# Kernel optimization log

Measured on AMD Instinct MI355X. Metric: run time of the kernel, lower is better.

## Reference

```python
import jax, jax.numpy as jnp
import numpy as np

H, INNER, V = 64, 32, 64
LR = 0.05
B, L = 256, 2048


def setup_inputs() -> dict:
    key = jax.random.key(0)
    ks = jax.random.split(key, 8)
    s = 0.05
    return {
        "seq":   jax.random.randint(ks[0], (B, L), 0, V),
        "embed": jax.random.normal(ks[1], (V, H), jnp.float32) * s,
        "ffw1":  jax.random.normal(ks[2], (2 * H, H), jnp.float32) * s,
        "ffb1":  jnp.zeros((2 * H,), jnp.float32),
        "ffw2":  jax.random.normal(ks[3], (H, 2 * H), jnp.float32) * s,
        "ffb2":  jnp.zeros((H,), jnp.float32),
        "ln_g":  jnp.ones((H,), jnp.float32),
        "ln_b":  jnp.zeros((H,), jnp.float32),
        "w1":    jax.random.normal(ks[4], (INNER, H), jnp.float32) * s,
        "b1":    jnp.zeros((INNER,), jnp.float32),
        "w2":    jax.random.normal(ks[5], (H, INNER), jnp.float32) * s,
        "b2":    jnp.zeros((H,), jnp.float32),
        "wout":  jax.random.normal(ks[6], (V, H), jnp.float32) * s,
        "bout":  jnp.zeros((V,), jnp.float32),
    }


def _encoder(seq, embed, ffw1, ffb1, ffw2, ffb2, ln_g, ln_b):
    e = embed[seq]                                             # [B,L,H]
    ff = jnp.maximum(e @ ffw1.T + ffb1, 0.0) @ ffw2.T + ffb2   # [B,L,H]
    x = e + ff
    mu = x.mean(-1, keepdims=True)
    var = x.var(-1, keepdims=True)                             # biased, like nn.LayerNorm
    return (x - mu) / jnp.sqrt(var + 1e-5) * ln_g + ln_b


def _ttt_one(kseq, vseq, last, w1, b1, w2, b2):
    # Sequential inner-loop TTT: per (k,v) pair, one SGD step on the tiny MLP
    # with analytic gradients of MSE(pred, v) (mean over H).
    def step(carry, kv):
        w1c, b1c, w2c, b2c = carry
        k, v = kv
        pre = w1c @ k + b1c                # [INNER]
        h = jnp.maximum(pre, 0.0)
        pred = w2c @ h + b2c               # [H]
        d = (2.0 / H) * (pred - v)         # dL/dpred
        gw2 = jnp.outer(d, h)
        gb2 = d
        dh = (w2c.T @ d) * (pre > 0.0)
        gw1 = jnp.outer(dh, k)
        gb1 = dh
        return (w1c - LR * gw1, b1c - LR * gb1,
                w2c - LR * gw2, b2c - LR * gb2), None

    (w1f, b1f, w2f, b2f), _ = jax.lax.scan(step, (w1, b1, w2, b2), (kseq, vseq))
    return w2f @ jnp.maximum(w1f @ last + b1f, 0.0) + b2f


def reference(seq, embed, ffw1, ffb1, ffw2, ffb2, ln_g, ln_b,
              w1, b1, w2, b2, wout, bout):
    hs = _encoder(seq, embed, ffw1, ffb1, ffw2, ffb2, ln_g, ln_b)
    hs = jax.lax.stop_gradient(hs)         # torch detaches kh/vh/last
    Lc = hs.shape[1]
    nsteps = (Lc - 2) // 2                 # len(range(0, L-3, 2))
    kseq = hs[:, 0:Lc - 3:2]               # [B,nsteps,H]
    vseq = hs[:, 1:Lc - 2:2][:, :nsteps]   # [B,nsteps,H]
    w1_0 = jax.lax.stop_gradient(w1)
    b1_0 = jax.lax.stop_gradient(b1)
    w2_0 = jax.lax.stop_gradient(w2)
    b2_0 = jax.lax.stop_gradient(b2)
    ctxs = jax.vmap(_ttt_one, in_axes=(0, 0, 0, None, None, None, None))(
        kseq, vseq, hs[:, -1], w1_0, b1_0, w2_0, b2_0)  # [B,H]
    return ctxs @ wout.T + bout            # [B,V]
```

## Files before the change

### kernel.cpp

```cpp
#include <hip/hip_runtime.h>

#define HD 64
#define VOCAB 64
#define BATCH 256
#define SEQLEN 2048
#define NSTEPS ((SEQLEN - 2) / 2)
#define LRc 0.05f

typedef __attribute__((ext_vector_type(2))) float f2;

__device__ __forceinline__ float xsum32(float x) {
  unsigned int u = __float_as_uint(x);
  auto r = __builtin_amdgcn_permlane32_swap(u, u, false, false);
  return __uint_as_float(r[0]) + __uint_as_float(r[1]);
}

__device__ __forceinline__ void pk_fma_s(f2& acc, const f2& w, const f2& shp) {
  asm("v_pk_fma_f32 %0, %2, %1, %0" : "+v"(acc) : "v"(w), "s"(shp));
}

__global__ __launch_bounds__(64, 1) void enc_build(
    const float* __restrict__ embed, const float* __restrict__ ffw1,
    const float* __restrict__ ffb1, const float* __restrict__ ffw2,
    const float* __restrict__ ffb2, const float* __restrict__ ln_g,
    const float* __restrict__ ln_b, float* __restrict__ enc) {
  const int v = blockIdx.x, j = threadIdx.x;
  __shared__ float e_s[HD];
  __shared__ float hid_s[2 * HD];
  float e = embed[v * HD + j];
  e_s[j] = e;
  __syncthreads();
  float ha = ffb1[j], hb = ffb1[HD + j];
  #pragma unroll 8
  for (int h = 0; h < HD; ++h) {
    float eh = e_s[h];
    ha = fmaf(ffw1[j * HD + h], eh, ha);
    hb = fmaf(ffw1[(HD + j) * HD + h], eh, hb);
  }
  hid_s[j] = fmaxf(ha, 0.f);
  hid_s[HD + j] = fmaxf(hb, 0.f);
  __syncthreads();
  float ff = ffb2[j];
  #pragma unroll 8
  for (int h2 = 0; h2 < 2 * HD; ++h2) ff = fmaf(ffw2[j * 2 * HD + h2], hid_s[h2], ff);
  float x = e + ff;
  float mu = x;
  #pragma unroll
  for (int m = 1; m < 64; m <<= 1) mu += __shfl_xor(mu, m, 64);
  mu *= (1.f / 64.f);
  float xc = x - mu;
  float var = xc * xc;
  #pragma unroll
  for (int m = 1; m < 64; m <<= 1) var += __shfl_xor(var, m, 64);
  var *= (1.f / 64.f);
  enc[v * HD + j] = xc / sqrtf(var + 1e-5f) * ln_g[j] + ln_b[j];
}

__global__ __launch_bounds__(64, 1) void gram_build(
    const float* __restrict__ enc, float* __restrict__ G) {
  __shared__ float es[VOCAB * HD];
  const int u = blockIdx.x, v = threadIdx.x;
  #pragma unroll
  for (int q = 0; q < 16; ++q)
    ((float4*)es)[v + 64 * q] = ((const float4*)enc)[v + 64 * q];
  __syncthreads();
  const float* a = &es[u * HD];
  const float* bb = &es[v * HD];
  float s0 = 0.f, s1 = 0.f, s2 = 0.f, s3 = 0.f;
  #pragma unroll
  for (int j = 0; j < HD; j += 4) {
    s0 = fmaf(a[j + 0], bb[j + 0], s0);
    s1 = fmaf(a[j + 1], bb[j + 1], s1);
    s2 = fmaf(a[j + 2], bb[j + 2], s2);
    s3 = fmaf(a[j + 3], bb[j + 3], s3);
  }
  G[u * VOCAB + v] = (s0 + s1) + (s2 + s3);
}

__device__ __forceinline__ void ttt_step(
    int l, int half,
    const float* __restrict__ enc_s, const float* __restrict__ G_s,
    const int* __restrict__ seq_s, float* __restrict__ sd_s,
    f2 (&W1)[16], f2 (&W2R2)[16], f2 (&W2T)[16],
    float& b1r, float& b2r,
    f2 (&KC)[16], float& vvC, f2 (&KN)[16], float& vvN,
    float& POFb, float& KKF, float& dhp,
    int2& tk, int2& tk1, int pidx) {
  float pre = fmaf(dhp, KKF, POFb);
  float h = fmaxf(pre, 0.f);

  const float* krn = &enc_s[tk1.x * HD + half * 32];
  float4* kn4 = (float4*)&KN[0];
  #pragma unroll
  for (int q = 0; q < 8; ++q) kn4[q] = *(const float4*)&krn[4 * q];
  vvN = enc_s[tk1.y * HD + l];
  float KKFn = G_s[tk.x * VOCAB + tk1.x];
  int2 tk2 = *(const int2*)&seq_s[pidx];

  f2 shp[16];
  #pragma unroll
  for (int c = 0; c < 16; ++c) {
    float a = __int_as_float(__builtin_amdgcn_readlane(__float_as_int(h), 2 * c));
    float bq = __int_as_float(__builtin_amdgcn_readlane(__float_as_int(h), 2 * c + 1));
    shp[c] = f2{a, bq};
  }

  f2 qa = {b2r, 0.f}, qb = {0.f, 0.f}, qc = {0.f, 0.f}, qd = {0.f, 0.f};
  #pragma unroll
  for (int c = 0; c < 16; c += 4) {
    pk_fma_s(qa, W2R2[c + 0], shp[c + 0]);
    pk_fma_s(qb, W2R2[c + 1], shp[c + 1]);
    pk_fma_s(qc, W2R2[c + 2], shp[c + 2]);
    pk_fma_s(qd, W2R2[c + 3], shp[c + 3]);
  }
  float pred = ((qa.x + qa.y) + (qb.x + qb.y)) + ((qc.x + qc.y) + (qd.x + qd.y));
  float sR = (vvC - pred) * (2.f * LRc / (float)HD);
  sd_s[l] = sR;

  f2 SD[16];
  {
    const float* drp = &sd_s[half * 32];
    float4* sd4 = (float4*)&SD[0];
    #pragma unroll
    for (int q = 0; q < 8; ++q) sd4[q] = *(const float4*)&drp[4 * q];
  }

  f2 sr2 = {sR, sR};
  #pragma unroll
  for (int c = 0; c < 16; ++c) pk_fma_s(W2R2[c], sr2, shp[c]);
  b2r += sR;
  f2 p0 = {0.f, 0.f}, p1 = {0.f, 0.f};
  #pragma unroll
  for (int c = 0; c < 16; c += 2) {
    p0 = __builtin_elementwise_fma(W1[c + 0], KN[c + 0], p0);
    p1 = __builtin_elementwise_fma(W1[c + 1], KN[c + 1], p1);
  }
  f2 ps = p0 + p1;
  float POFn = xsum32(ps.x + ps.y);
  float PB = POFn + b1r;

  f2 g0 = {0.f, 0.f}, g1 = {0.f, 0.f};
  #pragma unroll
  for (int r = 0; r < 16; r += 2) {
    g0 = __builtin_elementwise_fma(W2T[r + 0], SD[r + 0], g0);
    g1 = __builtin_elementwise_fma(W2T[r + 1], SD[r + 1], g1);
  }
  f2 gs = g0 + g1;
  float dh = xsum32(gs.x + gs.y);
  dh = (pre > 0.f) ? dh : 0.f;

  f2 h2 = {h, h};
  #pragma unroll
  for (int r = 0; r < 16; ++r) W2T[r] = __builtin_elementwise_fma(SD[r], h2, W2T[r]);
  f2 dh2 = {dh, dh};
  #pragma unroll
  for (int c = 0; c < 16; ++c) W1[c] = __builtin_elementwise_fma(dh2, KC[c], W1[c]);
  b1r += dh;

  POFb = PB + dh;
  KKF = KKFn;
  dhp = dh;
  tk = tk1;
  tk1 = tk2;
}

__global__ __launch_bounds__(64, 1) void ttt_run(
    const int* __restrict__ seq, const float* __restrict__ enc,
    const float* __restrict__ Gg,
    const float* __restrict__ w1g, const float* __restrict__ b1g,
    const float* __restrict__ w2g, const float* __restrict__ b2g,
    const float* __restrict__ woutg, const float* __restrict__ boutg,
    float* __restrict__ out) {
  __shared__ float enc_s[VOCAB * HD];
  __shared__ float G_s[VOCAB * VOCAB];
  __shared__ int   seq_s[SEQLEN];
  __shared__ float sd_s[64];
  __shared__ float ctx_s[64];
  const int b = blockIdx.x, l = threadIdx.x;
  const int i = l & 31, half = l >> 5;

  #pragma unroll
  for (int q = 0; q < 16; ++q)
    ((float4*)enc_s)[l + 64 * q] = ((const float4*)enc)[l + 64 * q];
  #pragma unroll
  for (int q = 0; q < 16; ++q)
    ((float4*)G_s)[l + 64 * q] = ((const float4*)Gg)[l + 64 * q];
  const int4* seqg = (const int4*)(seq + b * SEQLEN);
  #pragma unroll
  for (int q = 0; q < 8; ++q)
    ((int4*)seq_s)[l + 64 * q] = seqg[l + 64 * q];

  f2 W1[16], W2R2[16], W2T[16];
  {
    float4* w14 = (float4*)&W1[0];
    #pragma unroll
    for (int q = 0; q < 8; ++q) w14[q] = *(const float4*)&w1g[i * 64 + half * 32 + 4 * q];
    float4* w2r4 = (float4*)&W2R2[0];
    #pragma unroll
    for (int q = 0; q < 8; ++q) w2r4[q] = *(const float4*)&w2g[l * 32 + 4 * q];
  }
  #pragma unroll
  for (int r = 0; r < 16; ++r)
    W2T[r] = f2{w2g[(half * 32 + 2 * r) * 32 + i], w2g[(half * 32 + 2 * r + 1) * 32 + i]};
  float b1r = b1g[i];
  float b2r = b2g[l];
  __syncthreads();

  int2 tk  = *(const int2*)&seq_s[0];
  int2 tk1 = *(const int2*)&seq_s[2];
  f2 KA[16], KB[16];
  float vvA, vvB;
  {
    const float* kr = &enc_s[tk.x * HD + half * 32];
    float4* ka4 = (float4*)&KA[0];
    #pragma unroll
    for (int q = 0; q < 8; ++q) ka4[q] = *(const float4*)&kr[4 * q];
    vvA = enc_s[tk.y * HD + l];
  }
  float POFb, KKF = 0.f, dhp = 0.f;
  {
    f2 p0 = {0.f, 0.f}, p1 = {0.f, 0.f};
    #pragma unroll
    for (int c = 0; c < 16; c += 2) {
      p0 = __builtin_elementwise_fma(W1[c + 0], KA[c + 0], p0);
      p1 = __builtin_elementwise_fma(W1[c + 1], KA[c + 1], p1);
    }
    f2 ps = p0 + p1;
    POFb = xsum32(ps.x + ps.y) + b1r;
  }

  for (int s = 0; s < NSTEPS - 1; s += 2) {
    ttt_step(l, half, enc_s, G_s, seq_s, sd_s, W1, W2R2, W2T, b1r, b2r,
             KA, vvA, KB, vvB, POFb, KKF, dhp, tk, tk1, 2 * s + 4);
    ttt_step(l, half, enc_s, G_s, seq_s, sd_s, W1, W2R2, W2T, b1r, b2r,
             KB, vvB, KA, vvA, POFb, KKF, dhp, tk, tk1, 2 * s + 6);
  }
  ttt_step(l, half, enc_s, G_s, seq_s, sd_s, W1, W2R2, W2T, b1r, b2r,
           KA, vvA, KB, vvB, POFb, KKF, dhp, tk, tk1, 2046 );

  {
    int tok = seq_s[SEQLEN - 1];
    f2 K[16];
    const float* kr = &enc_s[tok * HD + half * 32];
    float4* k4 = (float4*)&K[0];
    #pragma unroll
    for (int q = 0; q < 8; ++q) k4[q] = *(const float4*)&kr[4 * q];
    f2 a0 = {0.f, 0.f}, a1 = {0.f, 0.f};
    #pragma unroll
    for (int c = 0; c < 16; c += 2) {
      a0 = __builtin_elementwise_fma(W1[c + 0], K[c + 0], a0);
      a1 = __builtin_elementwise_fma(W1[c + 1], K[c + 1], a1);
    }
    f2 as = a0 + a1;
    float pre = xsum32(as.x + as.y) + b1r;
    float h = fmaxf(pre, 0.f);
    f2 shp[16];
    #pragma unroll
    for (int c = 0; c < 16; ++c) {
      float aa = __int_as_float(__builtin_amdgcn_readlane(__float_as_int(h), 2 * c));
      float bb = __int_as_float(__builtin_amdgcn_readlane(__float_as_int(h), 2 * c + 1));
      shp[c] = f2{aa, bb};
    }
    f2 qa = {b2r, 0.f}, qb = {0.f, 0.f}, qc = {0.f, 0.f}, qd = {0.f, 0.f};
    #pragma unroll
    for (int c = 0; c < 16; c += 4) {
      pk_fma_s(qa, W2R2[c + 0], shp[c + 0]);
      pk_fma_s(qb, W2R2[c + 1], shp[c + 1]);
      pk_fma_s(qc, W2R2[c + 2], shp[c + 2]);
      pk_fma_s(qd, W2R2[c + 3], shp[c + 3]);
    }
    ctx_s[l] = ((qa.x + qa.y) + (qb.x + qb.y)) + ((qc.x + qc.y) + (qd.x + qd.y));
    __syncthreads();
    float acc = boutg[l];
    #pragma unroll 8
    for (int jj = 0; jj < 64; ++jj) acc = fmaf(woutg[l * 64 + jj], ctx_s[jj], acc);
    out[b * 64 + l] = acc;
  }
}

extern "C" void kernel_launch(void* const* d_in, const int* in_sizes, int n_in,
                              void* d_out, int out_size, void* d_ws, size_t ws_size,
                              hipStream_t stream) {
  const int*   seq   = (const int*)d_in[0];
  const float* embed = (const float*)d_in[1];
  const float* ffw1  = (const float*)d_in[2];
  const float* ffb1  = (const float*)d_in[3];
  const float* ffw2  = (const float*)d_in[4];
  const float* ffb2  = (const float*)d_in[5];
  const float* ln_g  = (const float*)d_in[6];
  const float* ln_b  = (const float*)d_in[7];
  const float* w1    = (const float*)d_in[8];
  const float* b1    = (const float*)d_in[9];
  const float* w2    = (const float*)d_in[10];
  const float* b2    = (const float*)d_in[11];
  const float* wout  = (const float*)d_in[12];
  const float* bout  = (const float*)d_in[13];
  float* enc = (float*)d_ws;
  float* G   = (float*)d_ws + 4096;

  enc_build<<<VOCAB, 64, 0, stream>>>(embed, ffw1, ffb1, ffw2, ffb2, ln_g, ln_b, enc);
  gram_build<<<VOCAB, 64, 0, stream>>>(enc, G);
  ttt_run<<<BATCH, 64, 0, stream>>>(seq, enc, G, w1, b1, w2, b2, wout, bout, (float*)d_out);
}
```

Baseline: 436.3 us.

## Defer weight updates one step and broadcast hidden activations via LDS

The W1 and W2T rank-1 updates for a step are postponed into the start of the next step, so they overlap with that step's independent loads and the forward dot products. A final W1 update is added after the loop. The 32 readlane scalar broadcasts of h are replaced by writing h to shared memory and reading it back as packed vectors, so the FMAs use VGPR operands instead of SGPRs. This shortens the serial critical path of each step but carries more live registers (SD, KX, hp) and an LDS round trip with no explicit barrier, relying on single-wave lockstep execution.

```diff
diff --git a/kernel.cpp b/kernel.cpp
--- a/kernel.cpp
+++ b/kernel.cpp
@@ -13,10 +13,6 @@
   unsigned int u = __float_as_uint(x);
   auto r = __builtin_amdgcn_permlane32_swap(u, u, false, false);
   return __uint_as_float(r[0]) + __uint_as_float(r[1]);
-}
-
-__device__ __forceinline__ void pk_fma_s(f2& acc, const f2& w, const f2& shp) {
-  asm("v_pk_fma_f32 %0, %2, %1, %0" : "+v"(acc) : "v"(w), "s"(shp));
 }
 
 __global__ __launch_bounds__(64, 1) void enc_build(
@@ -78,46 +74,56 @@
 }
 
 __device__ __forceinline__ void ttt_step(
-    int l, int half,
+    int l, int i, int half,
     const float* __restrict__ enc_s, const float* __restrict__ G_s,
     const int* __restrict__ seq_s, float* __restrict__ sd_s,
+    float* __restrict__ h_s,
     f2 (&W1)[16], f2 (&W2R2)[16], f2 (&W2T)[16],
     float& b1r, float& b2r,
-    f2 (&KC)[16], float& vvC, f2 (&KN)[16], float& vvN,
+    f2 (&KC)[16], float& vvC, f2 (&KX)[16], float& vvN,
+    f2 (&SD)[16], float& hp,
     float& POFb, float& KKF, float& dhp,
     int2& tk, int2& tk1, int pidx) {
   float pre = fmaf(dhp, KKF, POFb);
   float h = fmaxf(pre, 0.f);
 
+  h_s[i] = h;
+  f2 H2[16];
+  {
+    float4* h4 = (float4*)&H2[0];
+    #pragma unroll
+    for (int q = 0; q < 8; ++q) h4[q] = *(const float4*)&h_s[4 * q];
+  }
+
+  f2 dhp2 = {dhp, dhp};
+  #pragma unroll
+  for (int c = 0; c < 16; ++c) W1[c] = __builtin_elementwise_fma(dhp2, KX[c], W1[c]);
+
   const float* krn = &enc_s[tk1.x * HD + half * 32];
-  float4* kn4 = (float4*)&KN[0];
-  #pragma unroll
-  for (int q = 0; q < 8; ++q) kn4[q] = *(const float4*)&krn[4 * q];
+  float4* kx4 = (float4*)&KX[0];
+  #pragma unroll
+  for (int q = 0; q < 8; ++q) kx4[q] = *(const float4*)&krn[4 * q];
   vvN = enc_s[tk1.y * HD + l];
   float KKFn = G_s[tk.x * VOCAB + tk1.x];
   int2 tk2 = *(const int2*)&seq_s[pidx];
 
-  f2 shp[16];
-  #pragma unroll
-  for (int c = 0; c < 16; ++c) {
-    float a = __int_as_float(__builtin_amdgcn_readlane(__float_as_int(h), 2 * c));
-    float bq = __int_as_float(__builtin_amdgcn_readlane(__float_as_int(h), 2 * c + 1));
-    shp[c] = f2{a, bq};
-  }
+  f2 hp2 = {hp, hp};
+  #pragma unroll
+  for (int r = 0; r < 16; ++r) W2T[r] = __builtin_elementwise_fma(SD[r], hp2, W2T[r]);
 
   f2 qa = {b2r, 0.f}, qb = {0.f, 0.f}, qc = {0.f, 0.f}, qd = {0.f, 0.f};
   #pragma unroll
   for (int c = 0; c < 16; c += 4) {
-    pk_fma_s(qa, W2R2[c + 0], shp[c + 0]);
-    pk_fma_s(qb, W2R2[c + 1], shp[c + 1]);
-    pk_fma_s(qc, W2R2[c + 2], shp[c + 2]);
-    pk_fma_s(qd, W2R2[c + 3], shp[c + 3]);
-  }
-  float pred = ((qa.x + qa.y) + (qb.x + qb.y)) + ((qc.x + qc.y) + (qd.x + qd.y));
+    qa = __builtin_elementwise_fma(W2R2[c + 0], H2[c + 0], qa);
+    qb = __builtin_elementwise_fma(W2R2[c + 1], H2[c + 1], qb);
+    qc = __builtin_elementwise_fma(W2R2[c + 2], H2[c + 2], qc);
+    qd = __builtin_elementwise_fma(W2R2[c + 3], H2[c + 3], qd);
+  }
+  f2 qs = (qa + qb) + (qc + qd);
+  float pred = qs.x + qs.y;
   float sR = (vvC - pred) * (2.f * LRc / (float)HD);
   sd_s[l] = sR;
 
-  f2 SD[16];
   {
     const float* drp = &sd_s[half * 32];
     float4* sd4 = (float4*)&SD[0];
@@ -127,17 +133,16 @@
 
   f2 sr2 = {sR, sR};
   #pragma unroll
-  for (int c = 0; c < 16; ++c) pk_fma_s(W2R2[c], sr2, shp[c]);
+  for (int c = 0; c < 16; ++c) W2R2[c] = __builtin_elementwise_fma(sr2, H2[c], W2R2[c]);
   b2r += sR;
   f2 p0 = {0.f, 0.f}, p1 = {0.f, 0.f};
   #pragma unroll
   for (int c = 0; c < 16; c += 2) {
-    p0 = __builtin_elementwise_fma(W1[c + 0], KN[c + 0], p0);
-    p1 = __builtin_elementwise_fma(W1[c + 1], KN[c + 1], p1);
+    p0 = __builtin_elementwise_fma(W1[c + 0], KX[c + 0], p0);
+    p1 = __builtin_elementwise_fma(W1[c + 1], KX[c + 1], p1);
   }
   f2 ps = p0 + p1;
-  float POFn = xsum32(ps.x + ps.y);
-  float PB = POFn + b1r;
+  float PB = xsum32(ps.x + ps.y) + b1r;
 
   f2 g0 = {0.f, 0.f}, g1 = {0.f, 0.f};
   #pragma unroll
@@ -149,17 +154,11 @@
   float dh = xsum32(gs.x + gs.y);
   dh = (pre > 0.f) ? dh : 0.f;
 
-  f2 h2 = {h, h};
-  #pragma unroll
-  for (int r = 0; r < 16; ++r) W2T[r] = __builtin_elementwise_fma(SD[r], h2, W2T[r]);
-  f2 dh2 = {dh, dh};
-  #pragma unroll
-  for (int c = 0; c < 16; ++c) W1[c] = __builtin_elementwise_fma(dh2, KC[c], W1[c]);
   b1r += dh;
-
   POFb = PB + dh;
   KKF = KKFn;
   dhp = dh;
+  hp = h;
   tk = tk1;
   tk1 = tk2;
 }
@@ -175,6 +174,7 @@
   __shared__ float G_s[VOCAB * VOCAB];
   __shared__ int   seq_s[SEQLEN];
   __shared__ float sd_s[64];
+  __shared__ float h_s[32];
   __shared__ float ctx_s[64];
   const int b = blockIdx.x, l = threadIdx.x;
   const int i = l & 31, half = l >> 5;
@@ -208,7 +208,7 @@
 
   int2 tk  = *(const int2*)&seq_s[0];
   int2 tk1 = *(const int2*)&seq_s[2];
-  f2 KA[16], KB[16];
+  f2 KA[16], KB[16], SD[16];
   float vvA, vvB;
   {
     const float* kr = &enc_s[tk.x * HD + half * 32];
@@ -217,6 +217,10 @@
     for (int q = 0; q < 8; ++q) ka4[q] = *(const float4*)&kr[4 * q];
     vvA = enc_s[tk.y * HD + l];
   }
+  #pragma unroll
+  for (int c = 0; c < 16; ++c) { KB[c] = f2{0.f, 0.f}; SD[c] = f2{0.f, 0.f}; }
+  float hp = 0.f;
+
   float POFb, KKF = 0.f, dhp = 0.f;
   {
     f2 p0 = {0.f, 0.f}, p1 = {0.f, 0.f};
@@ -230,13 +234,19 @@
   }
 
   for (int s = 0; s < NSTEPS - 1; s += 2) {
-    ttt_step(l, half, enc_s, G_s, seq_s, sd_s, W1, W2R2, W2T, b1r, b2r,
-             KA, vvA, KB, vvB, POFb, KKF, dhp, tk, tk1, 2 * s + 4);
-    ttt_step(l, half, enc_s, G_s, seq_s, sd_s, W1, W2R2, W2T, b1r, b2r,
-             KB, vvB, KA, vvA, POFb, KKF, dhp, tk, tk1, 2 * s + 6);
-  }
-  ttt_step(l, half, enc_s, G_s, seq_s, sd_s, W1, W2R2, W2T, b1r, b2r,
-           KA, vvA, KB, vvB, POFb, KKF, dhp, tk, tk1, 2046 );
+    ttt_step(l, i, half, enc_s, G_s, seq_s, sd_s, h_s, W1, W2R2, W2T, b1r, b2r,
+             KA, vvA, KB, vvB, SD, hp, POFb, KKF, dhp, tk, tk1, 2 * s + 4);
+    ttt_step(l, i, half, enc_s, G_s, seq_s, sd_s, h_s, W1, W2R2, W2T, b1r, b2r,
+             KB, vvB, KA, vvA, SD, hp, POFb, KKF, dhp, tk, tk1, 2 * s + 6);
+  }
+  ttt_step(l, i, half, enc_s, G_s, seq_s, sd_s, h_s, W1, W2R2, W2T, b1r, b2r,
+           KA, vvA, KB, vvB, SD, hp, POFb, KKF, dhp, tk, tk1, 2046 );
+
+  {
+    f2 dhp2 = {dhp, dhp};
+    #pragma unroll
+    for (int c = 0; c < 16; ++c) W1[c] = __builtin_elementwise_fma(dhp2, KA[c], W1[c]);
+  }
 
   {
     int tok = seq_s[SEQLEN - 1];
@@ -254,22 +264,23 @@
     f2 as = a0 + a1;
     float pre = xsum32(as.x + as.y) + b1r;
     float h = fmaxf(pre, 0.f);
-    f2 shp[16];
-    #pragma unroll
-    for (int c = 0; c < 16; ++c) {
-      float aa = __int_as_float(__builtin_amdgcn_readlane(__float_as_int(h), 2 * c));
-      float bb = __int_as_float(__builtin_amdgcn_readlane(__float_as_int(h), 2 * c + 1));
-      shp[c] = f2{aa, bb};
+    h_s[i] = h;
+    f2 H2[16];
+    {
+      float4* h4 = (float4*)&H2[0];
+      #pragma unroll
+      for (int q = 0; q < 8; ++q) h4[q] = *(const float4*)&h_s[4 * q];
     }
     f2 qa = {b2r, 0.f}, qb = {0.f, 0.f}, qc = {0.f, 0.f}, qd = {0.f, 0.f};
     #pragma unroll
     for (int c = 0; c < 16; c += 4) {
-      pk_fma_s(qa, W2R2[c + 0], shp[c + 0]);
-      pk_fma_s(qb, W2R2[c + 1], shp[c + 1]);
-      pk_fma_s(qc, W2R2[c + 2], shp[c + 2]);
-      pk_fma_s(qd, W2R2[c + 3], shp[c + 3]);
+      qa = __builtin_elementwise_fma(W2R2[c + 0], H2[c + 0], qa);
+      qb = __builtin_elementwise_fma(W2R2[c + 1], H2[c + 1], qb);
+      qc = __builtin_elementwise_fma(W2R2[c + 2], H2[c + 2], qc);
+      qd = __builtin_elementwise_fma(W2R2[c + 3], H2[c + 3], qd);
     }
-    ctx_s[l] = ((qa.x + qa.y) + (qb.x + qb.y)) + ((qc.x + qc.y) + (qd.x + qd.y));
+    f2 qs = (qa + qb) + (qc + qd);
+    ctx_s[l] = qs.x + qs.y;
     __syncthreads();
     float acc = boutg[l];
     #pragma unroll 8
```

After: 380.3 us (median of 2 runs). 12.8% less time.
